# Kernel tuning notes

Hardware: AMD Instinct MI355X
Metric: run time of the kernel (lower is better)

## Reference

```python
import jax, jax.numpy as jnp
import numpy as np

DIM = 768
NUM_HEADS = 12
HEAD_DIM = DIM // NUM_HEADS
H = W = 64
RANK = 4
LORA_SCALING = 1.0 / RANK  # lora_alpha(=1) / r


def setup_inputs() -> dict:
    key = jax.random.key(0)
    ks = jax.random.split(key, 11)
    s = 0.02
    return {
        "x": jax.random.normal(ks[0], (1, H, W, DIM), dtype=jnp.float32),
        "W_qkv": jax.random.normal(ks[1], (3 * DIM, DIM), dtype=jnp.float32) * s,
        "b_qkv": jax.random.normal(ks[2], (3 * DIM,), dtype=jnp.float32) * s,
        "A_q": jax.random.normal(ks[3], (RANK, DIM), dtype=jnp.float32) * s,
        "B_q": jax.random.normal(ks[4], (DIM, RANK), dtype=jnp.float32) * s,
        "A_v": jax.random.normal(ks[5], (RANK, DIM), dtype=jnp.float32) * s,
        "B_v": jax.random.normal(ks[6], (DIM, RANK), dtype=jnp.float32) * s,
        "rel_h": jax.random.normal(ks[7], (2 * H - 1, HEAD_DIM), dtype=jnp.float32) * s,
        "rel_w": jax.random.normal(ks[8], (2 * W - 1, HEAD_DIM), dtype=jnp.float32) * s,
        "W_proj": jax.random.normal(ks[9], (DIM, DIM), dtype=jnp.float32) * s,
        "b_proj": jax.random.normal(ks[10], (DIM,), dtype=jnp.float32) * s,
    }


def _get_rel_pos(size, rel_pos):
    # q_size == k_size == size; relative coords indexed into (2*size-1, head_dim)
    coords = jnp.arange(size)[:, None] - jnp.arange(size)[None, :] + (size - 1)
    return rel_pos[coords]  # (size, size, head_dim)


def reference(x, W_qkv, b_qkv, A_q, B_q, A_v, B_v, rel_h, rel_w, W_proj, b_proj):
    B, h, w, dim = x.shape
    nh, hd = NUM_HEADS, HEAD_DIM
    scale = hd ** -0.5
    n = h * w
    xf = x.reshape(B, n, dim)

    # LoRA-merged QKV: base linear + low-rank deltas on q and v thirds only
    qkv = xf @ W_qkv.T + b_qkv  # (B, n, 3*dim)
    dq = ((xf @ A_q.T) @ B_q.T) * LORA_SCALING
    dv = ((xf @ A_v.T) @ B_v.T) * LORA_SCALING
    qkv = qkv.at[..., :dim].add(dq).at[..., 2 * dim:].add(dv)

    qkv = qkv.reshape(B, n, 3, nh, hd).transpose(2, 0, 3, 1, 4).reshape(3, B * nh, n, hd)
    q, k, v = qkv[0], qkv[1], qkv[2]  # each (B*nh, n, hd)

    attn = (q * scale) @ jnp.swapaxes(k, -2, -1)  # (B*nh, n, n)

    # decomposed relative position bias (SAM style)
    Rh = _get_rel_pos(h, rel_h)  # (h, h, hd)
    Rw = _get_rel_pos(w, rel_w)  # (w, w, hd)
    r_q = q.reshape(B * nh, h, w, hd)
    bias_h = jnp.einsum("bhwc,hkc->bhwk", r_q, Rh)  # (B*nh, h, w, h)
    bias_w = jnp.einsum("bhwc,wkc->bhwk", r_q, Rw)  # (B*nh, h, w, w)
    attn = (attn.reshape(B * nh, h, w, h, w)
            + bias_h[:, :, :, :, None]
            + bias_w[:, :, :, None, :]).reshape(B * nh, n, n)

    attn = jax.nn.softmax(attn, axis=-1)
    out = (attn @ v).reshape(B, nh, h, w, hd).transpose(0, 2, 3, 1, 4).reshape(B, h, w, dim)
    return out @ W_proj.T + b_proj
```

## Files before the change

### kernel.cpp

```cpp
#include <hip/hip_runtime.h>

#define NTOK 4096
#define DIMD 768
#define NHD  12
#define HDD  64
#define DK   800

typedef float  f32x2  __attribute__((ext_vector_type(2)));
typedef float  f32x4  __attribute__((ext_vector_type(4)));
typedef float  f32x16 __attribute__((ext_vector_type(16)));
typedef short  s16x8  __attribute__((ext_vector_type(8)));

#define MFMA16(a, b, c) __builtin_amdgcn_mfma_f32_16x16x32_bf16(a, b, c, 0, 0, 0)
#define MFMA32(a, b, c) __builtin_amdgcn_mfma_f32_32x32x16_bf16(a, b, c, 0, 0, 0)

#if __has_builtin(__builtin_amdgcn_exp2f)
#define EXP2(x) __builtin_amdgcn_exp2f(x)
#else
#define EXP2(x) exp2f(x)
#endif

__device__ inline short f2b(float f) {
  unsigned u = __float_as_uint(f);
  u += 0x7FFFu + ((u >> 16) & 1u);
  return (short)(u >> 16);
}
__device__ inline float b2f(short s) {
  return __uint_as_float(((unsigned)(unsigned short)s) << 16);
}
__device__ inline void gl_lds16(const short* g, short* l) {
  __builtin_amdgcn_global_load_lds(
      (const __attribute__((address_space(1))) unsigned int*)g,
      (__attribute__((address_space(3))) unsigned int*)l, 16, 0, 0);
}


__global__ __launch_bounds__(64)
void k_prep_w(const float* __restrict__ Wqkv, const float* __restrict__ Bq,
              const float* __restrict__ Bv, const float* __restrict__ Wp,
              short* __restrict__ we, short* __restrict__ wpb) {
  const int j = blockIdx.x;
  const int l = threadIdx.x;
  if (j < 2304) {
#pragma unroll
    for (int k = 0; k < 12; ++k)
      we[(size_t)j * DK + l + 64 * k] = f2b(Wqkv[(size_t)j * DIMD + l + 64 * k]);
    if (l < 32) {
      int c = 768 + l;
      short v = 0;
      if (l < 4) {
        if (j < 768) v = f2b(Bq[j * 4 + l]);
      } else if (l < 8) {
        if (j >= 1536) v = f2b(Bv[(j - 1536) * 4 + (l - 4)]);
      }
      we[(size_t)j * DK + c] = v;
    }
  } else {
    const int jr = j - 2304;
#pragma unroll
    for (int k = 0; k < 12; ++k)
      wpb[(size_t)jr * DIMD + l + 64 * k] =
          f2b(Wp[(size_t)jr * DIMD + l + 64 * k]);
  }
}

__global__ __launch_bounds__(64)
void k_prep_x(const float* __restrict__ x, const float* __restrict__ Aq,
              const float* __restrict__ Av, short* __restrict__ xe) {
  const int i = blockIdx.x;
  const int l = threadIdx.x;
  float xv[12];
#pragma unroll
  for (int k = 0; k < 12; ++k) xv[k] = x[(size_t)i * DIMD + l + 64 * k];
#pragma unroll
  for (int k = 0; k < 12; ++k)
    xe[(size_t)i * DK + l + 64 * k] = f2b(xv[k]);
  float a8[8];
#pragma unroll
  for (int o = 0; o < 8; ++o) {
    const float* A = (o < 4) ? (Aq + o * DIMD) : (Av + (o - 4) * DIMD);
    float acc = 0.f;
#pragma unroll
    for (int k = 0; k < 12; ++k) acc = fmaf(xv[k], A[l + 64 * k], acc);
#pragma unroll
    for (int off = 32; off; off >>= 1) acc += __shfl_xor(acc, off, 64);
    a8[o] = acc;
  }
  if (l < 32) {
    float v = 0.f;
#pragma unroll
    for (int o = 0; o < 8; ++o)
      if (l == o) v = 0.25f * a8[o];
    xe[(size_t)i * DK + 768 + l] = (l < 8) ? f2b(v) : (short)0;
  }
}

__global__ __launch_bounds__(256)
void k_qkv(const short* __restrict__ xe, const short* __restrict__ we,
           const float* __restrict__ bqkv, short* __restrict__ qkvb,
           short* __restrict__ vtb) {
  const int j0 = blockIdx.x * 128;
  const int i0 = blockIdx.y * 128;
  __shared__ short As[128 * 32];
  __shared__ short Bs[128 * 32];
  __shared__ short Cs[128 * 130];
  const int t = threadIdx.x, lane = t & 63, w = t >> 6;
  const int l15 = lane & 15, quad = lane >> 4;
  const int wm = w >> 1, wn = w & 1;

  f32x4 acc[4][4];
#pragma unroll
  for (int a = 0; a < 4; ++a)
#pragma unroll
    for (int b = 0; b < 4; ++b) acc[a][b] = (f32x4){0.f, 0.f, 0.f, 0.f};

  for (int kk = 0; kk < DK; kk += 32) {
    __syncthreads();
#pragma unroll
    for (int rep = 0; rep < 2; ++rep) {
      int c = rep * 256 + w * 64 + lane;
      gl_lds16(xe + (size_t)(i0 + (c >> 2)) * DK + kk + (c & 3) * 8,
               &As[(rep * 256 + w * 64) * 8]);
      gl_lds16(we + (size_t)(j0 + (c >> 2)) * DK + kk + (c & 3) * 8,
               &Bs[(rep * 256 + w * 64) * 8]);
    }
    __syncthreads();
    s16x8 af[4], bf[4];
#pragma unroll
    for (int mt = 0; mt < 4; ++mt)
      af[mt] = *(const s16x8*)&As[(wm * 64 + mt * 16 + l15) * 32 + quad * 8];
#pragma unroll
    for (int nt = 0; nt < 4; ++nt)
      bf[nt] = *(const s16x8*)&Bs[(wn * 64 + nt * 16 + l15) * 32 + quad * 8];
#pragma unroll
    for (int mt = 0; mt < 4; ++mt)
#pragma unroll
      for (int nt = 0; nt < 4; ++nt)
        acc[mt][nt] = MFMA16(af[mt], bf[nt], acc[mt][nt]);
  }

  const int which = j0 / DIMD;
  float bj[4];
#pragma unroll
  for (int nt = 0; nt < 4; ++nt) bj[nt] = bqkv[j0 + wn * 64 + nt * 16 + l15];

#pragma unroll
  for (int mt = 0; mt < 4; ++mt)
#pragma unroll
    for (int r = 0; r < 4; ++r) {
      const int row = wm * 64 + mt * 16 + quad * 4 + r;
#pragma unroll
      for (int nt = 0; nt < 4; ++nt) {
        const int col = wn * 64 + nt * 16 + l15;
        Cs[row * 130 + col] = f2b(acc[mt][nt][r] + bj[nt]);
      }
    }
  __syncthreads();
  const int base_head = (j0 - which * DIMD) >> 6;
  if (which != 2) {
#pragma unroll
    for (int rp = 0; rp < 8; ++rp) {
      int f = t + 256 * rp;
      int row = f >> 4, ch = f & 15;
      int head = base_head + (ch >> 3);
      int ddb = (ch & 7) * 8;
      s16x8 v = *(const s16x8*)&Cs[row * 130 + ch * 8];
      *(s16x8*)&qkvb[(((size_t)which * NHD + head) * NTOK + i0 + row) * HDD + ddb] = v;
    }
  } else {
#pragma unroll
    for (int rp = 0; rp < 8; ++rp) {
      int f = t + 256 * rp;
      int dcol = f >> 4, n8 = (f & 15) * 8;
      unsigned wds[4];
#pragma unroll
      for (int m = 0; m < 4; ++m) {
        int s0 = n8 + 2 * m, s1 = s0 + 1;
        int sr0 = (s0 & 0x70) | ((((s0 >> 2) & 3) == 1 ? 2 : ((s0 >> 2) & 3) == 2 ? 1 : ((s0 >> 2) & 3)) << 2) | (s0 & 3);
        int sr1 = (s1 & 0x70) | ((((s1 >> 2) & 3) == 1 ? 2 : ((s1 >> 2) & 3) == 2 ? 1 : ((s1 >> 2) & 3)) << 2) | (s1 & 3);
        unsigned lo = (unsigned short)Cs[sr0 * 130 + dcol];
        unsigned hi = (unsigned short)Cs[sr1 * 130 + dcol];
        wds[m] = lo | (hi << 16);
      }
      short* dst = vtb + ((size_t)(base_head * 64) + dcol) * NTOK + i0 + n8;
      *(int4*)dst = *(int4*)&wds[0];
    }
  }
}

__global__ __launch_bounds__(256)
void k_attn7(const short* __restrict__ qkvb, const short* __restrict__ vtb,
             const float* __restrict__ relh, const float* __restrict__ relw,
             short* __restrict__ attnb) {
  const int d_ = blockIdx.y * 64 + blockIdx.x;
  const int lin = (d_ & 7) * 96 + (d_ >> 3);
  const int head = lin >> 6;
  const int hq = lin & 63;
  const int n0 = hq * 64;

  __shared__ short sm[20480];
  short* smb = sm;

  const short* qg  = qkvb + (size_t)(0 * NHD + head) * NTOK * HDD;
  const short* kg  = qkvb + (size_t)(1 * NHD + head) * NTOK * HDD;
  const short* vtg = vtb + (size_t)head * HDD * NTOK;

  const int t = threadIdx.x;
  const int w = t >> 6, lane = t & 63;
  const int l31 = lane & 31, h = lane >> 5;
  const int kh = w >> 1, qh = w & 1;
  const int q = qh * 32 + l31;

  const int rowp = lane >> 1;
  const int cw = (w * 2 + (lane & 1)) * 8;
  const short* gK0 = kg + (size_t)rowp * HDD + cw;
  const short* gK1 = gK0 + 32 * HDD;
  const short* gV0 = vtg + (size_t)rowp * NTOK + cw;
  const short* gV1 = gV0 + (size_t)32 * NTOK;

  s16x8 qb[4];
#pragma unroll
  for (int s = 0; s < 4; ++s)
    qb[s] = *(const s16x8*)&qg[(size_t)(n0 + q) * HDD + s * 16 + 8 * h];

#pragma unroll
  for (int rp = 0; rp < 4; ++rp) {
    int f = t + 256 * rp;
    int d = f >> 3, c = (f & 7) * 8;
    float4 v0 = make_float4(0, 0, 0, 0), v1 = v0;
    if (d < 127) {
      const float* s_ = relw + (size_t)d * HDD + c;
      v0 = *(const float4*)s_; v1 = *(const float4*)(s_ + 4);
    }
    short4 b0, b1;
    b0.x = f2b(v0.x); b0.y = f2b(v0.y); b0.z = f2b(v0.z); b0.w = f2b(v0.w);
    b1.x = f2b(v1.x); b1.y = f2b(v1.y); b1.z = f2b(v1.z); b1.w = f2b(v1.w);
    *(short4*)&smb[d * 72 + c] = b0;
    *(short4*)&smb[d * 72 + c + 4] = b1;
  }
  __syncthreads();

  f32x16 mc0 = (f32x16)(0.f), mc1 = (f32x16)(0.f);
#pragma unroll
  for (int s = 0; s < 4; ++s) {
    s16x8 a0 = *(const s16x8*)&smb[((kh * 2) * 32 + l31) * 72 + s * 16 + 8 * h];
    s16x8 a1 = *(const s16x8*)&smb[((kh * 2 + 1) * 32 + l31) * 72 + s * 16 + 8 * h];
    mc0 = MFMA32(a0, qb[s], mc0);
    mc1 = MFMA32(a1, qb[s], mc1);
  }
  __syncthreads();
#pragma unroll
  for (int reg = 0; reg < 16; ++reg) {
    int dl = (reg & 3) + 8 * (reg >> 2) + 4 * h;
    smb[(kh * 64 + dl) * 64 + q] = f2b(mc0[reg] * 1.44269504f);
    smb[(kh * 64 + 32 + dl) * 64 + q] = f2b(mc1[reg] * 1.44269504f);
  }
  __syncthreads();

  f32x2 bw2[8];
#pragma unroll
  for (int i = 0; i < 8; ++i)
#pragma unroll
    for (int p = 0; p < 2; ++p) {
      int reg = 2 * i + p;
      int kl64 = kh * 32 + (reg & 3) + 8 * (reg >> 2) + 4 * h;
      int dneed = q - kl64 + 63;
      bw2[i][p] = b2f(smb[dneed * 64 + q]);
    }
  __syncthreads();

#pragma unroll
  for (int rp = 0; rp < 2; ++rp) {
    int f = t + 256 * rp;
    int kt = f >> 3, c = (f & 7) * 8;
    const float* s_ = relh + (size_t)(hq + 63 - kt) * HDD + c;
    float4 v0 = *(const float4*)s_, v1 = *(const float4*)(s_ + 4);
    short4 b0, b1;
    b0.x = f2b(v0.x); b0.y = f2b(v0.y); b0.z = f2b(v0.z); b0.w = f2b(v0.w);
    b1.x = f2b(v1.x); b1.y = f2b(v1.y); b1.z = f2b(v1.z); b1.w = f2b(v1.w);
    *(short4*)&smb[kt * 72 + c] = b0;
    *(short4*)&smb[kt * 72 + c + 4] = b1;
  }
  __syncthreads();

  f32x16 hc = (f32x16)(0.f);
#pragma unroll
  for (int s = 0; s < 4; ++s) {
    s16x8 a = *(const s16x8*)&smb[(kh * 32 + l31) * 72 + s * 16 + 8 * h];
    hc = MFMA32(a, qb[s], hc);
  }
#pragma unroll
  for (int reg = 0; reg < 16; ++reg) {
    int ktl = kh * 32 + (reg & 3) + 8 * (reg >> 2) + 4 * h;
    smb[16384 + ktl * 64 + q] = f2b(hc[reg] * 1.44269504f);
  }
  __syncthreads();

  gl_lds16(gK0, smb + 0 + w * 512);
  gl_lds16(gK1, smb + 2048 + w * 512);
  gl_lds16(gV0, smb + 8192 + w * 512);
  gl_lds16(gV1, smb + 8192 + 2048 + w * 512);
  gK0 += 4096; gK1 += 4096;
  gV0 += 64; gV1 += 64;

  int baseS[4], baseV[2];
#pragma unroll
  for (int s = 0; s < 4; ++s)
    baseS[s] = kh * 2048 + s * 512 + l31 * 16 + h * 8;
#pragma unroll
  for (int s2 = 0; s2 < 2; ++s2)
    baseV[s2] = (kh * 2 + s2) * 512 + l31 * 16 + h * 8;

  f32x2 ps2 = (f32x2)(0.f);
  f32x16 oc0 = (f32x16)(0.f), oc1 = (f32x16)(0.f);

#define ATTN_ITER(KT, KSRC, VSRC, KDST, VDST, DO_PF)                           \
  {                                                                            \
    __syncthreads();                                                           \
    if (DO_PF) {                                                               \
      gl_lds16(gK0, smb + (KDST) + w * 512);                                   \
      gl_lds16(gK1, smb + (KDST) + 2048 + w * 512);                            \
      gl_lds16(gV0, smb + (VDST) + w * 512);                                   \
      gl_lds16(gV1, smb + (VDST) + 2048 + w * 512);                            \
      gK0 += 4096; gK1 += 4096; gV0 += 64; gV1 += 64;                          \
    }                                                                          \
    f32x16 sc_ = (f32x16)(0.f);                                                \
    _Pragma("unroll") for (int s = 0; s < 4; ++s) {                            \
      s16x8 a = *(const s16x8*)&smb[(KSRC) + baseS[s]];                        \
      sc_ = MFMA32(a, qb[s], sc_);                                             \
    }                                                                          \
    float bhl2 = b2f(smb[16384 + (KT) * 64 + q]);                              \
    unsigned pk[8];                                                            \
    _Pragma("unroll") for (int i = 0; i < 8; ++i) {                            \
      f32x2 s2;                                                                \
      s2[0] = sc_[2 * i]; s2[1] = sc_[2 * i + 1];                              \
      f32x2 r = s2 * 0.18033688f + (bw2[i] + bhl2);                            \
      float e0 = EXP2(r[0]);                                                   \
      float e1 = EXP2(r[1]);                                                   \
      f32x2 e2; e2[0] = e0; e2[1] = e1;                                        \
      ps2 += e2;                                                               \
      pk[i] = __builtin_amdgcn_perm(__float_as_uint(e1),                       \
                                    __float_as_uint(e0), 0x07060302u);         \
    }                                                                          \
    _Pragma("unroll") for (int s2i = 0; s2i < 2; ++s2i) {                      \
      union { unsigned u[4]; s16x8 v; } B;                                     \
      B.u[0] = pk[4 * s2i + 0];                                                \
      B.u[1] = pk[4 * s2i + 1];                                                \
      B.u[2] = pk[4 * s2i + 2];                                                \
      B.u[3] = pk[4 * s2i + 3];                                                \
      s16x8 a0 = *(const s16x8*)&smb[(VSRC) + baseV[s2i]];                     \
      s16x8 a1 = *(const s16x8*)&smb[(VSRC) + 2048 + baseV[s2i]];              \
      oc0 = MFMA32(a0, B.v, oc0);                                              \
      oc1 = MFMA32(a1, B.v, oc1);                                              \
    }                                                                          \
  }

  for (int k2 = 0; k2 < 31; ++k2) {
    ATTN_ITER(2 * k2,     0,    8192,  4096, 12288, 1);
    ATTN_ITER(2 * k2 + 1, 4096, 12288, 0,    8192,  1);
  }
  ATTN_ITER(62, 0,    8192,  4096, 12288, 1);
  ATTN_ITER(63, 4096, 12288, 0,    8192,  0);
#undef ATTN_ITER

  __syncthreads();
  float ps = ps2[0] + ps2[1];
  float* obuf = (float*)smb;
  float* psb  = (float*)smb + 4224;
  short* tbuf = smb + 8576;
  ps += __shfl_xor(ps, 32, 64);
  if (kh == 1) {
#pragma unroll
    for (int reg = 0; reg < 16; ++reg) {
      int dl = (reg & 3) + 8 * (reg >> 2) + 4 * h;
      obuf[dl * 66 + q] = oc0[reg];
      obuf[(32 + dl) * 66 + q] = oc1[reg];
    }
    if (lane < 32) psb[q] = ps;
  }
  __syncthreads();
  if (kh == 0) {
    float inv = 1.f / (ps + psb[q]);
#pragma unroll
    for (int reg = 0; reg < 16; ++reg) {
      int dl = (reg & 3) + 8 * (reg >> 2) + 4 * h;
      tbuf[dl * 66 + q] = f2b((oc0[reg] + obuf[dl * 66 + q]) * inv);
      tbuf[(32 + dl) * 66 + q] = f2b((oc1[reg] + obuf[(32 + dl) * 66 + q]) * inv);
    }
  }
  __syncthreads();
  {
    int qq = t >> 2, seg = t & 3;
    unsigned wds[8];
#pragma unroll
    for (int m = 0; m < 8; ++m) {
      unsigned lo = (unsigned short)tbuf[(seg * 16 + 2 * m) * 66 + qq];
      unsigned hi = (unsigned short)tbuf[(seg * 16 + 2 * m + 1) * 66 + qq];
      wds[m] = lo | (hi << 16);
    }
    short* dst = attnb + (size_t)(n0 + qq) * DIMD + head * 64 + seg * 16;
    *(int4*)dst = *(int4*)&wds[0];
    *(int4*)(dst + 8) = *(int4*)&wds[4];
  }
}

__global__ __launch_bounds__(256)
void k_proj(const short* __restrict__ ab, const short* __restrict__ wpb,
            const float* __restrict__ bp, float* __restrict__ out) {
  const int j0 = blockIdx.x * 64;
  const int i0 = blockIdx.y * 128;
  __shared__ short As[128 * 32];
  __shared__ short Bs[64 * 32];
  const int t = threadIdx.x, lane = t & 63, w = t >> 6;
  const int l15 = lane & 15, quad = lane >> 4;
  const int wm = w >> 1, wn = w & 1;

  f32x4 acc[4][2];
#pragma unroll
  for (int a = 0; a < 4; ++a)
#pragma unroll
    for (int b = 0; b < 2; ++b) acc[a][b] = (f32x4){0.f, 0.f, 0.f, 0.f};

  for (int kk = 0; kk < DIMD; kk += 32) {
    __syncthreads();
#pragma unroll
    for (int rep = 0; rep < 2; ++rep) {
      int c = rep * 256 + w * 64 + lane;
      gl_lds16(ab + (size_t)(i0 + (c >> 2)) * DIMD + kk + (c & 3) * 8,
               &As[(rep * 256 + w * 64) * 8]);
    }
    {
      gl_lds16(wpb + (size_t)(j0 + ((w * 64 + lane) >> 2)) * DIMD + kk +
                   ((w * 64 + lane) & 3) * 8,
               &Bs[(w * 64) * 8]);
    }
    __syncthreads();
    s16x8 af[4], bf[2];
#pragma unroll
    for (int mt = 0; mt < 4; ++mt)
      af[mt] = *(const s16x8*)&As[(wm * 64 + mt * 16 + l15) * 32 + quad * 8];
#pragma unroll
    for (int nt = 0; nt < 2; ++nt)
      bf[nt] = *(const s16x8*)&Bs[(wn * 32 + nt * 16 + l15) * 32 + quad * 8];
#pragma unroll
    for (int mt = 0; mt < 4; ++mt)
#pragma unroll
      for (int nt = 0; nt < 2; ++nt)
        acc[mt][nt] = MFMA16(af[mt], bf[nt], acc[mt][nt]);
  }

#pragma unroll
  for (int mt = 0; mt < 4; ++mt)
#pragma unroll
    for (int r = 0; r < 4; ++r) {
      const int i = i0 + wm * 64 + mt * 16 + quad * 4 + r;
#pragma unroll
      for (int nt = 0; nt < 2; ++nt) {
        const int j = j0 + wn * 32 + nt * 16 + l15;
        out[(size_t)i * DIMD + j] = acc[mt][nt][r] + bp[j];
      }
    }
}

extern "C" void kernel_launch(void* const* d_in, const int* in_sizes, int n_in,
                              void* d_out, int out_size, void* d_ws, size_t ws_size,
                              hipStream_t stream) {
  (void)in_sizes; (void)n_in; (void)out_size; (void)ws_size;
  const float* x    = (const float*)d_in[0];
  const float* Wqkv = (const float*)d_in[1];
  const float* bqkv = (const float*)d_in[2];
  const float* Aq   = (const float*)d_in[3];
  const float* Bq   = (const float*)d_in[4];
  const float* Av   = (const float*)d_in[5];
  const float* Bv   = (const float*)d_in[6];
  const float* relh = (const float*)d_in[7];
  const float* relw = (const float*)d_in[8];
  const float* Wp   = (const float*)d_in[9];
  const float* bp   = (const float*)d_in[10];
  float* out = (float*)d_out;

  float* ws = (float*)d_ws;
  short* xe    = (short*)(ws);
  short* we    = (short*)(ws + 1638400);
  short* wpb   = (short*)(ws + 2560000);
  short* qkvb  = (short*)(ws + 2854912);
  short* vtb   = (short*)(ws + 7573504);
  short* attnb = (short*)(ws + 9146368);

  k_prep_w<<<dim3(3072), dim3(64), 0, stream>>>(Wqkv, Bq, Bv, Wp, we, wpb);
  k_prep_x<<<dim3(NTOK), dim3(64), 0, stream>>>(x, Aq, Av, xe);
  k_qkv<<<dim3(18, 32), dim3(256), 0, stream>>>(xe, we, bqkv, qkvb, vtb);
  k_attn7<<<dim3(64, NHD), dim3(256), 0, stream>>>(qkvb, vtb, relh, relw, attnb);
  k_proj<<<dim3(12, 32), dim3(256), 0, stream>>>(attnb, wpb, bp, out);
}
```

Baseline: 226.0 us.

## Software-pipeline attention softmax with PV, widen QKV k-tile, remap block order

The attention loop is restructured so each iteration computes the next tile's scores and exponentials while the PV MFMAs consume the previous tile's packed probabilities, letting matrix and transcendental work overlap. The QKV GEMM now uses 64-wide K steps with an XOR-swizzled LDS layout, handles the LoRA tail columns separately, and shares one LDS buffer between the input tiles and the output staging. Both the QKV and projection kernels remap block indices into XCD-interleaved order to improve L2 locality. This raises register pressure and loop complexity, and the block remap assumes a fixed grid size.

Measured after the change: 224.0 us. Within noise of the previous version (-0.9%).

```diff
diff --git a/kernel.cpp b/kernel.cpp
--- a/kernel.cpp
+++ b/kernel.cpp
@@ -99,11 +99,16 @@
 void k_qkv(const short* __restrict__ xe, const short* __restrict__ we,
            const float* __restrict__ bqkv, short* __restrict__ qkvb,
            short* __restrict__ vtb) {
-  const int j0 = blockIdx.x * 128;
-  const int i0 = blockIdx.y * 128;
-  __shared__ short As[128 * 32];
-  __shared__ short Bs[128 * 32];
-  __shared__ short Cs[128 * 130];
+  const int d_ = blockIdx.y * 18 + blockIdx.x;
+  const int lin = (d_ & 7) * 72 + (d_ >> 3);
+  const int j0 = (lin % 18) * 128;
+  const int i0 = (lin / 18) * 128;
+
+  __shared__ __align__(16) short shm[16640];
+  short* As = shm;
+  short* Bs = shm + 8192;
+  short* Cs = shm;
+
   const int t = threadIdx.x, lane = t & 63, w = t >> 6;
   const int l15 = lane & 15, quad = lane >> 4;
   const int wm = w >> 1, wn = w & 1;
@@ -114,17 +119,52 @@
 #pragma unroll
     for (int b = 0; b < 4; ++b) acc[a][b] = (f32x4){0.f, 0.f, 0.f, 0.f};
 
-  for (int kk = 0; kk < DK; kk += 32) {
+  for (int kk = 0; kk < 768; kk += 64) {
     __syncthreads();
 #pragma unroll
-    for (int rep = 0; rep < 2; ++rep) {
+    for (int rep = 0; rep < 4; ++rep) {
       int c = rep * 256 + w * 64 + lane;
-      gl_lds16(xe + (size_t)(i0 + (c >> 2)) * DK + kk + (c & 3) * 8,
+      int row = c >> 3, u = (c & 7) ^ (row & 7);
+      gl_lds16(xe + (size_t)(i0 + row) * DK + kk + u * 8,
                &As[(rep * 256 + w * 64) * 8]);
-      gl_lds16(we + (size_t)(j0 + (c >> 2)) * DK + kk + (c & 3) * 8,
+      gl_lds16(we + (size_t)(j0 + row) * DK + kk + u * 8,
                &Bs[(rep * 256 + w * 64) * 8]);
     }
     __syncthreads();
+#pragma unroll
+    for (int kh2 = 0; kh2 < 2; ++kh2) {
+      s16x8 af[4], bf[4];
+#pragma unroll
+      for (int mt = 0; mt < 4; ++mt) {
+        int row = wm * 64 + mt * 16 + l15;
+        af[mt] = *(const s16x8*)&As[row * 64 +
+                                    (((kh2 * 4 + quad) ^ (l15 & 7)) * 8)];
+      }
+#pragma unroll
+      for (int nt = 0; nt < 4; ++nt) {
+        int row = wn * 64 + nt * 16 + l15;
+        bf[nt] = *(const s16x8*)&Bs[row * 64 +
+                                    (((kh2 * 4 + quad) ^ (l15 & 7)) * 8)];
+      }
+#pragma unroll
+      for (int mt = 0; mt < 4; ++mt)
+#pragma unroll
+        for (int nt = 0; nt < 4; ++nt)
+          acc[mt][nt] = MFMA16(af[mt], bf[nt], acc[mt][nt]);
+    }
+  }
+
+  __syncthreads();
+#pragma unroll
+  for (int rep = 0; rep < 2; ++rep) {
+    int c = rep * 256 + w * 64 + lane;
+    gl_lds16(xe + (size_t)(i0 + (c >> 2)) * DK + 768 + (c & 3) * 8,
+             &As[(rep * 256 + w * 64) * 8]);
+    gl_lds16(we + (size_t)(j0 + (c >> 2)) * DK + 768 + (c & 3) * 8,
+             &Bs[(rep * 256 + w * 64) * 8]);
+  }
+  __syncthreads();
+  {
     s16x8 af[4], bf[4];
 #pragma unroll
     for (int mt = 0; mt < 4; ++mt)
@@ -138,6 +178,7 @@
       for (int nt = 0; nt < 4; ++nt)
         acc[mt][nt] = MFMA16(af[mt], bf[nt], acc[mt][nt]);
   }
+  __syncthreads();
 
   const int which = j0 / DIMD;
   float bj[4];
@@ -298,10 +339,13 @@
 
   gl_lds16(gK0, smb + 0 + w * 512);
   gl_lds16(gK1, smb + 2048 + w * 512);
+  gK0 += 4096; gK1 += 4096;
   gl_lds16(gV0, smb + 8192 + w * 512);
   gl_lds16(gV1, smb + 8192 + 2048 + w * 512);
+  gV0 += 64; gV1 += 64;
+  gl_lds16(gK0, smb + 4096 + w * 512);
+  gl_lds16(gK1, smb + 4096 + 2048 + w * 512);
   gK0 += 4096; gK1 += 4096;
-  gV0 += 64; gV1 += 64;
 
   int baseS[4], baseV[2];
 #pragma unroll
@@ -313,24 +357,62 @@
 
   f32x2 ps2 = (f32x2)(0.f);
   f32x16 oc0 = (f32x16)(0.f), oc1 = (f32x16)(0.f);
-
-#define ATTN_ITER(KT, KSRC, VSRC, KDST, VDST, DO_PF)                           \
+  unsigned pkA[8], pkB[8];
+
+  __syncthreads();
+
+  {
+    f32x16 sc_ = (f32x16)(0.f);
+#pragma unroll
+    for (int s = 0; s < 4; ++s) {
+      s16x8 a = *(const s16x8*)&smb[0 + baseS[s]];
+      sc_ = MFMA32(a, qb[s], sc_);
+    }
+    float bhl2 = b2f(smb[16384 + 0 * 64 + q]);
+#pragma unroll
+    for (int i = 0; i < 8; ++i) {
+      f32x2 s2;
+      s2[0] = sc_[2 * i]; s2[1] = sc_[2 * i + 1];
+      f32x2 r = s2 * 0.18033688f + (bw2[i] + bhl2);
+      float e0 = EXP2(r[0]);
+      float e1 = EXP2(r[1]);
+      f32x2 e2; e2[0] = e0; e2[1] = e1;
+      ps2 += e2;
+      pkA[i] = __builtin_amdgcn_perm(__float_as_uint(e1),
+                                     __float_as_uint(e0), 0x07060302u);
+    }
+  }
+
+#define ITER_P(KTN, VOFF, KOFFN, KDST, VDST, PFK, PFV, PKC, PKN)               \
   {                                                                            \
     __syncthreads();                                                           \
-    if (DO_PF) {                                                               \
+    if (PFK) {                                                                 \
       gl_lds16(gK0, smb + (KDST) + w * 512);                                   \
       gl_lds16(gK1, smb + (KDST) + 2048 + w * 512);                            \
+      gK0 += 4096; gK1 += 4096;                                                \
+    }                                                                          \
+    if (PFV) {                                                                 \
       gl_lds16(gV0, smb + (VDST) + w * 512);                                   \
       gl_lds16(gV1, smb + (VDST) + 2048 + w * 512);                            \
-      gK0 += 4096; gK1 += 4096; gV0 += 64; gV1 += 64;                          \
+      gV0 += 64; gV1 += 64;                                                    \
     }                                                                          \
     f32x16 sc_ = (f32x16)(0.f);                                                \
     _Pragma("unroll") for (int s = 0; s < 4; ++s) {                            \
-      s16x8 a = *(const s16x8*)&smb[(KSRC) + baseS[s]];                        \
+      s16x8 a = *(const s16x8*)&smb[(KOFFN) + baseS[s]];                       \
       sc_ = MFMA32(a, qb[s], sc_);                                             \
     }                                                                          \
-    float bhl2 = b2f(smb[16384 + (KT) * 64 + q]);                              \
-    unsigned pk[8];                                                            \
+    _Pragma("unroll") for (int s2i = 0; s2i < 2; ++s2i) {                      \
+      union { unsigned u[4]; s16x8 v; } B;                                     \
+      B.u[0] = PKC[4 * s2i + 0];                                               \
+      B.u[1] = PKC[4 * s2i + 1];                                               \
+      B.u[2] = PKC[4 * s2i + 2];                                               \
+      B.u[3] = PKC[4 * s2i + 3];                                               \
+      s16x8 a0 = *(const s16x8*)&smb[(VOFF) + baseV[s2i]];                     \
+      s16x8 a1 = *(const s16x8*)&smb[(VOFF) + 2048 + baseV[s2i]];              \
+      oc0 = MFMA32(a0, B.v, oc0);                                              \
+      oc1 = MFMA32(a1, B.v, oc1);                                              \
+    }                                                                          \
+    float bhl2 = b2f(smb[16384 + (KTN) * 64 + q]);                             \
     _Pragma("unroll") for (int i = 0; i < 8; ++i) {                            \
       f32x2 s2;                                                                \
       s2[0] = sc_[2 * i]; s2[1] = sc_[2 * i + 1];                              \
@@ -339,29 +421,30 @@
       float e1 = EXP2(r[1]);                                                   \
       f32x2 e2; e2[0] = e0; e2[1] = e1;                                        \
       ps2 += e2;                                                               \
-      pk[i] = __builtin_amdgcn_perm(__float_as_uint(e1),                       \
-                                    __float_as_uint(e0), 0x07060302u);         \
+      PKN[i] = __builtin_amdgcn_perm(__float_as_uint(e1),                      \
+                                     __float_as_uint(e0), 0x07060302u);        \
     }                                                                          \
-    _Pragma("unroll") for (int s2i = 0; s2i < 2; ++s2i) {                      \
-      union { unsigned u[4]; s16x8 v; } B;                                     \
-      B.u[0] = pk[4 * s2i + 0];                                                \
-      B.u[1] = pk[4 * s2i + 1];                                                \
-      B.u[2] = pk[4 * s2i + 2];                                                \
-      B.u[3] = pk[4 * s2i + 3];                                                \
-      s16x8 a0 = *(const s16x8*)&smb[(VSRC) + baseV[s2i]];                     \
-      s16x8 a1 = *(const s16x8*)&smb[(VSRC) + 2048 + baseV[s2i]];              \
-      oc0 = MFMA32(a0, B.v, oc0);                                              \
-      oc1 = MFMA32(a1, B.v, oc1);                                              \
-    }                                                                          \
-  }
-
-  for (int k2 = 0; k2 < 31; ++k2) {
-    ATTN_ITER(2 * k2,     0,    8192,  4096, 12288, 1);
-    ATTN_ITER(2 * k2 + 1, 4096, 12288, 0,    8192,  1);
-  }
-  ATTN_ITER(62, 0,    8192,  4096, 12288, 1);
-  ATTN_ITER(63, 4096, 12288, 0,    8192,  0);
-#undef ATTN_ITER
+  }
+
+  for (int m = 0; m < 31; ++m) {
+    ITER_P(2 * m + 1, 8192, 4096, 0, 12288, 1, 1, pkA, pkB);
+    ITER_P(2 * m + 2, 12288, 0, 4096, 8192, 1, 1, pkB, pkA);
+  }
+  ITER_P(63, 8192, 4096, 0, 12288, 0, 1, pkA, pkB);
+  __syncthreads();
+#pragma unroll
+  for (int s2i = 0; s2i < 2; ++s2i) {
+    union { unsigned u[4]; s16x8 v; } B;
+    B.u[0] = pkB[4 * s2i + 0];
+    B.u[1] = pkB[4 * s2i + 1];
+    B.u[2] = pkB[4 * s2i + 2];
+    B.u[3] = pkB[4 * s2i + 3];
+    s16x8 a0 = *(const s16x8*)&smb[12288 + baseV[s2i]];
+    s16x8 a1 = *(const s16x8*)&smb[12288 + 2048 + baseV[s2i]];
+    oc0 = MFMA32(a0, B.v, oc0);
+    oc1 = MFMA32(a1, B.v, oc1);
+  }
+#undef ITER_P
 
   __syncthreads();
   float ps = ps2[0] + ps2[1];
@@ -407,8 +490,10 @@
 __global__ __launch_bounds__(256)
 void k_proj(const short* __restrict__ ab, const short* __restrict__ wpb,
             const float* __restrict__ bp, float* __restrict__ out) {
-  const int j0 = blockIdx.x * 64;
-  const int i0 = blockIdx.y * 128;
+  const int d_ = blockIdx.y * 12 + blockIdx.x;
+  const int lin = (d_ & 7) * 48 + (d_ >> 3);
+  const int j0 = (lin % 12) * 64;
+  const int i0 = (lin / 12) * 128;
   __shared__ short As[128 * 32];
   __shared__ short Bs[64 * 32];
   const int t = threadIdx.x, lane = t & 63, w = t >> 6;
```
